# Optimization experiments

Hardware: AMD Instinct MI355X
Metric: run time of the kernel (lower is better)

Reference implementation:

```python
import jax, jax.numpy as jnp
import numpy as np

B, S, HID = 2, 2048, 1024
H, KVH = 16, 4           # query heads, kv heads
D = HID // H             # head_dim = 64
G = H // KVH             # group size (n_rep) = 4


def setup_inputs() -> dict:
    key = jax.random.key(0)
    ks = jax.random.split(key, 6)
    x = jax.random.normal(ks[0], (B, S, HID), dtype=jnp.float32)
    # RoPE tables: [S, D], standard theta=10000
    inv_freq = 1.0 / (10000.0 ** (jnp.arange(0, D, 2, dtype=jnp.float32) / D))
    freqs = jnp.arange(S, dtype=jnp.float32)[:, None] * inv_freq[None, :]  # [S, D/2]
    emb = jnp.concatenate([freqs, freqs], axis=-1)  # [S, D]
    cos, sin = jnp.cos(emb), jnp.sin(emb)
    scale = 0.02
    wq = jax.random.normal(ks[1], (HID, H * D), dtype=jnp.float32) * scale
    wk = jax.random.normal(ks[2], (HID, KVH * D), dtype=jnp.float32) * scale
    wv = jax.random.normal(ks[3], (HID, KVH * D), dtype=jnp.float32) * scale
    wo = jax.random.normal(ks[4], (H * D, HID), dtype=jnp.float32) * scale
    return {"x": x, "cos": cos, "sin": sin, "wq": wq, "wk": wk, "wv": wv, "wo": wo}


def _rotate_half(t):
    h = t.shape[-1] // 2
    return jnp.concatenate([-t[..., h:], t[..., :h]], axis=-1)


def reference(x, cos, sin, wq, wk, wv, wo):
    b, s, _ = x.shape
    q = (x @ wq).reshape(b, s, H, D)
    k = (x @ wk).reshape(b, s, KVH, D)
    v = (x @ wv).reshape(b, s, KVH, D)
    # RoPE (cos/sin broadcast over heads, unsqueeze_dim=1 -> [S,1,D])
    c = cos[:s, None, :]
    sn = sin[:s, None, :]
    q = q * c + _rotate_half(q) * sn
    k = k * c + _rotate_half(k) * sn
    # GQA attention without materializing repeated K/V: group q heads by kv head
    qg = q.reshape(b, s, KVH, G, D)
    scores = jnp.einsum('bqkgd,bskd->bkgqs', qg, k) / jnp.sqrt(jnp.asarray(D, q.dtype))
    causal = jnp.tril(jnp.ones((s, s), dtype=bool))  # [S_q, S_k]
    scores = jnp.where(causal[None, None, None, :, :], scores, -jnp.inf)
    p = jax.nn.softmax(scores, axis=-1)
    out = jnp.einsum('bkgqs,bskd->bqkgd', p, v).reshape(b, s, H * D)
    return out @ wo
```

## Files before the change

### kernel.cpp

```cpp
#include <hip/hip_runtime.h>
#include <hip/hip_bf16.h>


typedef short bfx8 __attribute__((ext_vector_type(8)));
typedef float fx4  __attribute__((ext_vector_type(4)));
typedef float fx16 __attribute__((ext_vector_type(16)));
typedef unsigned int ux4 __attribute__((ext_vector_type(4)));

#define DEV __device__ __forceinline__
#define ALPHA 0.18033688011112042f

DEV void load_lds16(const void* g, void* l) {
  __builtin_amdgcn_global_load_lds(
      (const __attribute__((address_space(1))) unsigned int*)g,
      (__attribute__((address_space(3))) unsigned int*)l, 16, 0, 0);
}

DEV unsigned short f2bf(float f) {
  unsigned int x = __builtin_bit_cast(unsigned int, f);
  unsigned int r = (x + 0x7fffu + ((x >> 16) & 1u)) >> 16;
  return (unsigned short)r;
}
DEV float bf2f(unsigned short u) {
  unsigned int x = ((unsigned int)u) << 16;
  return __builtin_bit_cast(float, x);
}
DEV float exp2_fast(float x) { float r; asm("v_exp_f32 %0, %1" : "=v"(r) : "v"(x)); return r; }
DEV unsigned cvtpk(float lo, float hi) {
  unsigned r; asm("v_cvt_pk_bf16_f32 %0, %1, %2" : "=v"(r) : "v"(lo), "v"(hi)); return r;
}


__global__ __launch_bounds__(256) void cvt_x_kernel(const float* __restrict__ x,
                                                    unsigned short* __restrict__ out) {
  int i = (blockIdx.x * 256 + threadIdx.x) * 8;
  fx4 a = *(const fx4*)(x + i);
  fx4 b = *(const fx4*)(x + i + 4);
  bfx8 r;
  r[0] = (short)f2bf(a[0]); r[1] = (short)f2bf(a[1]);
  r[2] = (short)f2bf(a[2]); r[3] = (short)f2bf(a[3]);
  r[4] = (short)f2bf(b[0]); r[5] = (short)f2bf(b[1]);
  r[6] = (short)f2bf(b[2]); r[7] = (short)f2bf(b[3]);
  *(bfx8*)(out + i) = r;
}


__global__ __launch_bounds__(256) void twqkv_kernel(const float* __restrict__ wq,
                                                    const float* __restrict__ wk,
                                                    const float* __restrict__ wv,
                                                    unsigned short* __restrict__ out) {
  __shared__ float tile[64 * 65];
  const int r0 = blockIdx.x * 64;
  const int c0 = blockIdx.y * 64;
  const float* src; int ncols, rofs;
  if (r0 < 1024)      { src = wq; ncols = 1024; rofs = r0; }
  else if (r0 < 1280) { src = wk; ncols = 256;  rofs = r0 - 1024; }
  else                { src = wv; ncols = 256;  rofs = r0 - 1280; }
  const int t = threadIdx.x;
#pragma unroll
  for (int p = 0; p < 4; ++p) {
    int idx = p * 256 + t;
    int cc = idx >> 4, q4 = idx & 15;
    fx4 v = *(const fx4*)(src + (size_t)(c0 + cc) * ncols + rofs + q4 * 4);
#pragma unroll
    for (int i = 0; i < 4; ++i) tile[(q4 * 4 + i) * 65 + cc] = v[i];
  }
  __syncthreads();
#pragma unroll
  for (int p = 0; p < 2; ++p) {
    int idx = p * 256 + t;
    int rr = idx >> 3, c8 = idx & 7;
    bfx8 v8;
#pragma unroll
    for (int i = 0; i < 8; ++i) v8[i] = (short)f2bf(tile[rr * 65 + c8 * 8 + i]);
    *(bfx8*)(out + (size_t)(r0 + rr) * 1024 + c0 + c8 * 8) = v8;
  }
}

__global__ __launch_bounds__(256) void two_kernel(const float* __restrict__ wo,
                                                  unsigned short* __restrict__ out) {
  __shared__ float tile[64 * 65];
  const int r0 = blockIdx.x * 64, c0 = blockIdx.y * 64;
  const int t = threadIdx.x;
#pragma unroll
  for (int p = 0; p < 4; ++p) {
    int idx = p * 256 + t;
    int cc = idx >> 4, q4 = idx & 15;
    fx4 v = *(const fx4*)(wo + (size_t)(c0 + cc) * 1024 + r0 + q4 * 4);
#pragma unroll
    for (int i = 0; i < 4; ++i) tile[(q4 * 4 + i) * 65 + cc] = v[i];
  }
  __syncthreads();
#pragma unroll
  for (int p = 0; p < 2; ++p) {
    int idx = p * 256 + t;
    int rr = idx >> 3, c8 = idx & 7;
    bfx8 v8;
#pragma unroll
    for (int i = 0; i < 8; ++i) v8[i] = (short)f2bf(tile[rr * 65 + c8 * 8 + i]);
    *(bfx8*)(out + (size_t)(r0 + rr) * 1024 + c0 + c8 * 8) = v8;
  }
}


__global__ __launch_bounds__(256) void vt_kernel(const unsigned short* __restrict__ qkv,
                                                 unsigned short* __restrict__ vT) {
  __shared__ __align__(16) unsigned short tile[64][72];
  const int sc = blockIdx.x;
  const int kvh = blockIdx.y, b = blockIdx.z;
  const int t = threadIdx.x;
  const unsigned short* src = qkv + ((size_t)b * 2048 + sc * 64) * 1536 + 1280 + kvh * 64;
#pragma unroll
  for (int p = 0; p < 2; ++p) {
    int idx = p * 256 + t;
    int row = idx >> 3, c = idx & 7;
    *(bfx8*)(&tile[row][c * 8]) = *(const bfx8*)(src + (size_t)row * 1536 + c * 8);
  }
  __syncthreads();
  unsigned short* dst = vT + ((size_t)(b * 4 + kvh) * 64) * 2048 + sc * 64;
#pragma unroll
  for (int p = 0; p < 2; ++p) {
    int idx = p * 256 + t;
    int d = idx >> 3, c = idx & 7;
    bfx8 v;
#pragma unroll
    for (int i = 0; i < 8; ++i) v[i] = (short)tile[c * 8 + i][d];
    *(bfx8*)(dst + (size_t)d * 2048 + c * 8) = v;
  }
}


template <bool OUT_BF16, bool FUSE_ROPE>
__global__ __launch_bounds__(256) void gemm_bt_kernel(const unsigned short* __restrict__ A,
                                                      const unsigned short* __restrict__ Bt,
                                                      void* __restrict__ Cp,
                                                      int M, int N, int K, int ldc,
                                                      const float* __restrict__ ct,
                                                      const float* __restrict__ st) {
  __shared__ __align__(16) unsigned short As[128 * 32];
  __shared__ __align__(16) unsigned short Bs[128 * 32];
  const int t = threadIdx.x;
  const int l = t & 63;
  const int w = t >> 6;
  const int wm = (w >> 1) * 64, wn = (w & 1) * 64;
  const int bm = blockIdx.x, bn = blockIdx.y;
  fx4 acc[4][4] = {};

  const int ra = t >> 2;
  const int ca = t & 3;

  for (int kt = 0; kt < K; kt += 32) {
    __syncthreads();
#pragma unroll
    for (int p = 0; p < 2; ++p) {
      int rr = ra + p * 64;
      int gca = ((ca ^ ((rr >> 1) & 3)) * 8);
      load_lds16(A + (size_t)(bm * 128 + rr) * K + kt + gca, (char*)As + p * 4096 + t * 16);
      load_lds16(Bt + (size_t)(bn * 128 + rr) * K + kt + gca, (char*)Bs + p * 4096 + t * 16);
    }
    __syncthreads();

    bfx8 af[4], bfr[4];
#pragma unroll
    for (int mi = 0; mi < 4; ++mi) {
      int row = wm + mi * 16 + (l & 15);
      int ch = (l >> 4) ^ ((row >> 1) & 3);
      af[mi] = *(const bfx8*)(As + row * 32 + ch * 8);
      int rowb = wn + mi * 16 + (l & 15);
      int chb = (l >> 4) ^ ((rowb >> 1) & 3);
      bfr[mi] = *(const bfx8*)(Bs + rowb * 32 + chb * 8);
    }
#pragma unroll
    for (int mi = 0; mi < 4; ++mi)
#pragma unroll
      for (int ni = 0; ni < 4; ++ni)
        acc[mi][ni] = __builtin_amdgcn_mfma_f32_16x16x32_bf16(af[mi], bfr[ni], acc[mi][ni], 0, 0, 0);
  }

  const int colbase = bn * 128 + wn;
  if (FUSE_ROPE && colbase < 1280) {
    const float qsc = (colbase < 1024) ? ALPHA : 1.0f;
    unsigned short* Cb = (unsigned short*)Cp;
#pragma unroll
    for (int mi = 0; mi < 4; ++mi) {
      int row0 = bm * 128 + wm + mi * 16 + (l >> 4) * 4;
#pragma unroll
      for (int r = 0; r < 4; ++r) {
        int row = row0 + r, s = row & 2047;
#pragma unroll
        for (int ni = 0; ni < 2; ++ni) {
          int d = ni * 16 + (l & 15);
          float c = ct[s * 64 + d], sn = st[s * 64 + d];
          float x0 = acc[mi][ni][r], x1 = acc[mi][ni + 2][r];
          Cb[(size_t)row * ldc + colbase + d]      = f2bf((x0 * c - x1 * sn) * qsc);
          Cb[(size_t)row * ldc + colbase + d + 32] = f2bf((x1 * c + x0 * sn) * qsc);
        }
      }
    }
  } else {
#pragma unroll
    for (int mi = 0; mi < 4; ++mi) {
      int row0 = bm * 128 + wm + mi * 16 + (l >> 4) * 4;
#pragma unroll
      for (int ni = 0; ni < 4; ++ni) {
        int col = colbase + ni * 16 + (l & 15);
#pragma unroll
        for (int r = 0; r < 4; ++r) {
          if (OUT_BF16)
            ((unsigned short*)Cp)[(size_t)(row0 + r) * ldc + col] = f2bf(acc[mi][ni][r]);
          else
            ((float*)Cp)[(size_t)(row0 + r) * ldc + col] = acc[mi][ni][r];
        }
      }
    }
  }
}


struct Frag { bfx8 kf[4]; bfx8 vf[4]; };

__global__ __launch_bounds__(64) void attn_kernel(const unsigned short* __restrict__ qkv,
                                                  const unsigned short* __restrict__ vT,
                                                  unsigned short* __restrict__ out) {
  __shared__ unsigned Ost[32 * 33];
  const int fid = blockIdx.x;
  const int pid = fid & 31;
  const int uu = fid >> 5;
  const int head = uu & 15, b = uu >> 4;
  const int kvh = head >> 2;
  const int l = threadIdx.x, q5 = l & 31, h = l >> 5;
  const size_t bbase = (size_t)b * 2048;
  const unsigned short* base = qkv + bbase * 1536;
  const unsigned short* kptr = base + 1024 + kvh * 64 + (size_t)q5 * 1536 + 8 * h;
  const unsigned short* vptr = vT + ((size_t)(b * 4 + kvh) * 64 + q5) * 2048 + 8 * h;

  Frag fA, fB;

#define LOADF(F, KB) do {                                                        \
    const unsigned short* kq = kptr + (size_t)(KB) * (32 * 1536);                \
    F.kf[0] = *(const bfx8*)(kq);                                                \
    F.kf[1] = *(const bfx8*)(kq + 16);                                           \
    F.kf[2] = *(const bfx8*)(kq + 32);                                           \
    F.kf[3] = *(const bfx8*)(kq + 48);                                           \
    const unsigned short* vq = vptr + (KB) * 32;                                 \
    F.vf[0] = *(const bfx8*)(vq);                                                \
    F.vf[1] = *(const bfx8*)(vq + 32 * 2048);                                    \
    F.vf[2] = *(const bfx8*)(vq + 16);                                           \
    F.vf[3] = *(const bfx8*)(vq + 16 + 32 * 2048);                               \
  } while (0)

#define STEP(F, KB) do {                                                         \
    fx16 s = {};                                                                 \
    s = __builtin_amdgcn_mfma_f32_32x32x16_bf16(F.kf[0], qf[0], s, 0, 0, 0);     \
    s = __builtin_amdgcn_mfma_f32_32x32x16_bf16(F.kf[1], qf[1], s, 0, 0, 0);     \
    s = __builtin_amdgcn_mfma_f32_32x32x16_bf16(F.kf[2], qf[2], s, 0, 0, 0);     \
    s = __builtin_amdgcn_mfma_f32_32x32x16_bf16(F.kf[3], qf[3], s, 0, 0, 0);     \
    if ((KB) == Tp) {                                                            \
      _Pragma("unroll")                                                          \
      for (int r = 0; r < 16; ++r) {                                             \
        int kr = (r & 3) + 8 * (r >> 2) + 4 * h;                                 \
        if (kr > q5) s[r] = -1e30f;                                              \
      }                                                                          \
    }                                                                            \
    float pmax = s[0];                                                           \
    _Pragma("unroll")                                                            \
    for (int r = 1; r < 16; ++r) pmax = fmaxf(pmax, s[r]);                       \
    pmax = fmaxf(pmax, __shfl_xor(pmax, 32, 64));                                \
    if (!__all(pmax <= mrun + 8.0f)) {                                           \
      float mnew = fmaxf(mrun, pmax);                                            \
      float corr = exp2_fast(mrun - mnew);                                       \
      mrun = mnew;                                                               \
      lrun *= corr;                                                              \
      o[0] *= corr; o[1] *= corr;                                                \
    }                                                                            \
    float lt = 0.f;                                                              \
    _Pragma("unroll")                                                            \
    for (int r = 0; r < 16; ++r) { float pv = exp2_fast(s[r] - mrun); s[r] = pv; lt += pv; } \
    lt += __shfl_xor(lt, 32, 64);                                                \
    lrun += lt;                                                                  \
    unsigned U[8];                                                               \
    _Pragma("unroll")                                                            \
    for (int k8 = 0; k8 < 8; ++k8) U[k8] = cvtpk(s[2 * k8], s[2 * k8 + 1]);      \
    _Pragma("unroll")                                                            \
    for (int kc = 0; kc < 2; ++kc) {                                             \
      unsigned send0 = h ? U[4 * kc] : U[4 * kc + 2];                            \
      unsigned send1 = h ? U[4 * kc + 1] : U[4 * kc + 3];                        \
      unsigned r0 = (unsigned)__shfl_xor((int)send0, 32, 64);                    \
      unsigned r1 = (unsigned)__shfl_xor((int)send1, 32, 64);                    \
      unsigned k0 = h ? U[4 * kc + 2] : U[4 * kc];                               \
      unsigned k1 = h ? U[4 * kc + 3] : U[4 * kc + 1];                           \
      ux4 fr;                                                                    \
      fr[0] = h ? r0 : k0; fr[1] = h ? r1 : k1;                                  \
      fr[2] = h ? k0 : r0; fr[3] = h ? k1 : r1;                                  \
      bfx8 pf = __builtin_bit_cast(bfx8, fr);                                    \
      o[0] = __builtin_amdgcn_mfma_f32_32x32x16_bf16(F.vf[kc * 2], pf, o[0], 0, 0, 0);     \
      o[1] = __builtin_amdgcn_mfma_f32_32x32x16_bf16(F.vf[kc * 2 + 1], pf, o[1], 0, 0, 0); \
    }                                                                            \
  } while (0)

#pragma unroll 1
  for (int sel = 0; sel < 2; ++sel) {
    const int Tp = sel ? (63 - pid) : pid;
    const int q0 = Tp * 32;
    const int nkb = Tp + 1;

    bfx8 qf[4];
#pragma unroll
    for (int dd = 0; dd < 4; ++dd)
      qf[dd] = *(const bfx8*)(base + (size_t)(q0 + q5) * 1536 + head * 64 + dd * 16 + 8 * h);

    fx16 o[2] = {};
    float mrun = -1e30f, lrun = 0.f;

    LOADF(fA, 0);
    int kb = 0;
    while (true) {
      if (kb + 1 < nkb) LOADF(fB, kb + 1);
      STEP(fA, kb);
      ++kb; if (kb >= nkb) break;
      if (kb + 1 < nkb) LOADF(fA, kb + 1);
      STEP(fB, kb);
      ++kb; if (kb >= nkb) break;
    }

    __syncthreads();
    float inv = 1.0f / lrun;
#pragma unroll
    for (int dt = 0; dt < 2; ++dt)
#pragma unroll
      for (int rp = 0; rp < 8; ++rp) {
        int r = 2 * rp;
        float a = o[dt][r] * inv, bb = o[dt][r + 1] * inv;
        int d = 32 * dt + (r & 3) + 8 * (r >> 2) + 4 * h;
        Ost[q5 * 33 + (d >> 1)] = cvtpk(a, bb);
      }
    __syncthreads();
    {
      int rr = l >> 1, half = l & 1;
      const unsigned* src = Ost + rr * 33 + half * 16;
      unsigned short* dst = out + (bbase + q0 + rr) * 1024 + head * 64 + half * 32;
#pragma unroll
      for (int u2 = 0; u2 < 4; ++u2) {
        ux4 v4;
        v4[0] = src[4 * u2]; v4[1] = src[4 * u2 + 1];
        v4[2] = src[4 * u2 + 2]; v4[3] = src[4 * u2 + 3];
        *(ux4*)(dst + u2 * 8) = v4;
      }
    }
  }
#undef LOADF
#undef STEP
}


extern "C" void kernel_launch(void* const* d_in, const int* in_sizes, int n_in,
                              void* d_out, int out_size, void* d_ws, size_t ws_size,
                              hipStream_t stream) {
  const float* x    = (const float*)d_in[0];
  const float* cosb = (const float*)d_in[1];
  const float* sinb = (const float*)d_in[2];
  const float* wq   = (const float*)d_in[3];
  const float* wk   = (const float*)d_in[4];
  const float* wv   = (const float*)d_in[5];
  const float* wo   = (const float*)d_in[6];
  float* out = (float*)d_out;

  char* ws = (char*)d_ws;
  unsigned short* xb    = (unsigned short*)ws;
  unsigned short* attn  = (unsigned short*)ws;
  unsigned short* wqkvT = (unsigned short*)(ws + 8388608);
  unsigned short* vT    = (unsigned short*)(ws + 8388608);
  unsigned short* woT   = (unsigned short*)(ws + 11534336);
  unsigned short* qkv   = (unsigned short*)(ws + 13631488);

  cvt_x_kernel<<<2048, 256, 0, stream>>>(x, xb);
  twqkv_kernel<<<dim3(24, 16), 256, 0, stream>>>(wq, wk, wv, wqkvT);
  two_kernel<<<dim3(16, 16), 256, 0, stream>>>(wo, woT);
  gemm_bt_kernel<true, true><<<dim3(32, 12), 256, 0, stream>>>(xb, wqkvT, qkv, 4096, 1536, 1024, 1536, cosb, sinb);
  vt_kernel<<<dim3(32, 4, 2), 256, 0, stream>>>(qkv, vT);
  attn_kernel<<<1024, 64, 0, stream>>>(qkv, vT, attn);
  gemm_bt_kernel<false, false><<<dim3(32, 8), 256, 0, stream>>>(attn, woT, out, 4096, 1024, 1024, 1024, nullptr, nullptr);
}
```

Before: 210.2 us.

## Fuse weight transposes, write V transposed from QKV GEMM, restructure attention blocks

Merges the two weight-transpose kernels into one launch. The QKV GEMM epilogue now writes V directly in transposed layout, which removes the separate vt kernel and shrinks the qkv row stride to 1280. GEMM tiles are halved in M (64x128) to double the grid. Attention now runs one query tile per workgroup, 2048 workgroups in heaviest-first order, processes 64-key blocks with two score accumulators and s_setprio around MFMAs, and drops a barrier. The risks are more workgroups with less reuse per block and higher register pressure in attention.

```diff
diff --git a/kernel.cpp b/kernel.cpp
--- a/kernel.cpp
+++ b/kernel.cpp
@@ -2,6 +2,7 @@
 #include <hip/hip_bf16.h>
 
 
+typedef short bfx4 __attribute__((ext_vector_type(4)));
 typedef short bfx8 __attribute__((ext_vector_type(8)));
 typedef float fx4  __attribute__((ext_vector_type(4)));
 typedef float fx16 __attribute__((ext_vector_type(16)));
@@ -21,14 +22,11 @@
   unsigned int r = (x + 0x7fffu + ((x >> 16) & 1u)) >> 16;
   return (unsigned short)r;
 }
-DEV float bf2f(unsigned short u) {
-  unsigned int x = ((unsigned int)u) << 16;
-  return __builtin_bit_cast(float, x);
-}
 DEV float exp2_fast(float x) { float r; asm("v_exp_f32 %0, %1" : "=v"(r) : "v"(x)); return r; }
 DEV unsigned cvtpk(float lo, float hi) {
   unsigned r; asm("v_cvt_pk_bf16_f32 %0, %1, %2" : "=v"(r) : "v"(lo), "v"(hi)); return r;
 }
+#define MFMA32 __builtin_amdgcn_mfma_f32_32x32x16_bf16
 
 
 __global__ __launch_bounds__(256) void cvt_x_kernel(const float* __restrict__ x,
@@ -45,17 +43,24 @@
 }
 
 
-__global__ __launch_bounds__(256) void twqkv_kernel(const float* __restrict__ wq,
-                                                    const float* __restrict__ wk,
-                                                    const float* __restrict__ wv,
-                                                    unsigned short* __restrict__ out) {
+__global__ __launch_bounds__(256) void tw_kernel(const float* __restrict__ wq,
+                                                 const float* __restrict__ wk,
+                                                 const float* __restrict__ wv,
+                                                 const float* __restrict__ wo,
+                                                 unsigned short* __restrict__ wqkvT,
+                                                 unsigned short* __restrict__ woT) {
   __shared__ float tile[64 * 65];
-  const int r0 = blockIdx.x * 64;
+  const int bx = blockIdx.x;
   const int c0 = blockIdx.y * 64;
-  const float* src; int ncols, rofs;
-  if (r0 < 1024)      { src = wq; ncols = 1024; rofs = r0; }
-  else if (r0 < 1280) { src = wk; ncols = 256;  rofs = r0 - 1024; }
-  else                { src = wv; ncols = 256;  rofs = r0 - 1280; }
+  const float* src; int ncols, rofs, r0; unsigned short* dst;
+  if (bx < 24) {
+    r0 = bx * 64; dst = wqkvT;
+    if (r0 < 1024)      { src = wq; ncols = 1024; rofs = r0; }
+    else if (r0 < 1280) { src = wk; ncols = 256;  rofs = r0 - 1024; }
+    else                { src = wv; ncols = 256;  rofs = r0 - 1280; }
+  } else {
+    r0 = (bx - 24) * 64; dst = woT; src = wo; ncols = 1024; rofs = r0;
+  }
   const int t = threadIdx.x;
 #pragma unroll
   for (int p = 0; p < 4; ++p) {
@@ -73,59 +78,7 @@
     bfx8 v8;
 #pragma unroll
     for (int i = 0; i < 8; ++i) v8[i] = (short)f2bf(tile[rr * 65 + c8 * 8 + i]);
-    *(bfx8*)(out + (size_t)(r0 + rr) * 1024 + c0 + c8 * 8) = v8;
-  }
-}
-
-__global__ __launch_bounds__(256) void two_kernel(const float* __restrict__ wo,
-                                                  unsigned short* __restrict__ out) {
-  __shared__ float tile[64 * 65];
-  const int r0 = blockIdx.x * 64, c0 = blockIdx.y * 64;
-  const int t = threadIdx.x;
-#pragma unroll
-  for (int p = 0; p < 4; ++p) {
-    int idx = p * 256 + t;
-    int cc = idx >> 4, q4 = idx & 15;
-    fx4 v = *(const fx4*)(wo + (size_t)(c0 + cc) * 1024 + r0 + q4 * 4);
-#pragma unroll
-    for (int i = 0; i < 4; ++i) tile[(q4 * 4 + i) * 65 + cc] = v[i];
-  }
-  __syncthreads();
-#pragma unroll
-  for (int p = 0; p < 2; ++p) {
-    int idx = p * 256 + t;
-    int rr = idx >> 3, c8 = idx & 7;
-    bfx8 v8;
-#pragma unroll
-    for (int i = 0; i < 8; ++i) v8[i] = (short)f2bf(tile[rr * 65 + c8 * 8 + i]);
-    *(bfx8*)(out + (size_t)(r0 + rr) * 1024 + c0 + c8 * 8) = v8;
-  }
-}
-
-
-__global__ __launch_bounds__(256) void vt_kernel(const unsigned short* __restrict__ qkv,
-                                                 unsigned short* __restrict__ vT) {
-  __shared__ __align__(16) unsigned short tile[64][72];
-  const int sc = blockIdx.x;
-  const int kvh = blockIdx.y, b = blockIdx.z;
-  const int t = threadIdx.x;
-  const unsigned short* src = qkv + ((size_t)b * 2048 + sc * 64) * 1536 + 1280 + kvh * 64;
-#pragma unroll
-  for (int p = 0; p < 2; ++p) {
-    int idx = p * 256 + t;
-    int row = idx >> 3, c = idx & 7;
-    *(bfx8*)(&tile[row][c * 8]) = *(const bfx8*)(src + (size_t)row * 1536 + c * 8);
-  }
-  __syncthreads();
-  unsigned short* dst = vT + ((size_t)(b * 4 + kvh) * 64) * 2048 + sc * 64;
-#pragma unroll
-  for (int p = 0; p < 2; ++p) {
-    int idx = p * 256 + t;
-    int d = idx >> 3, c = idx & 7;
-    bfx8 v;
-#pragma unroll
-    for (int i = 0; i < 8; ++i) v[i] = (short)tile[c * 8 + i][d];
-    *(bfx8*)(dst + (size_t)d * 2048 + c * 8) = v;
+    *(bfx8*)(dst + (size_t)(r0 + rr) * 1024 + c0 + c8 * 8) = v8;
   }
 }
 
@@ -134,44 +87,50 @@
 __global__ __launch_bounds__(256) void gemm_bt_kernel(const unsigned short* __restrict__ A,
                                                       const unsigned short* __restrict__ Bt,
                                                       void* __restrict__ Cp,
-                                                      int M, int N, int K, int ldc,
+                                                      int K, int ldc,
                                                       const float* __restrict__ ct,
-                                                      const float* __restrict__ st) {
-  __shared__ __align__(16) unsigned short As[128 * 32];
+                                                      const float* __restrict__ st,
+                                                      unsigned short* __restrict__ vTout) {
+  __shared__ __align__(16) unsigned short As[64 * 32];
   __shared__ __align__(16) unsigned short Bs[128 * 32];
   const int t = threadIdx.x;
   const int l = t & 63;
   const int w = t >> 6;
-  const int wm = (w >> 1) * 64, wn = (w & 1) * 64;
+  const int wm = (w >> 1) * 32, wn = (w & 1) * 64;
   const int bm = blockIdx.x, bn = blockIdx.y;
-  fx4 acc[4][4] = {};
-
-  const int ra = t >> 2;
-  const int ca = t & 3;
+  fx4 acc[2][4] = {};
 
   for (int kt = 0; kt < K; kt += 32) {
     __syncthreads();
+    {
+      int rr = t >> 2, ca = t & 3;
+      int gca = ((ca ^ ((rr >> 1) & 3)) * 8);
+      load_lds16(A + (size_t)(bm * 64 + rr) * K + kt + gca, (char*)As + t * 16);
+    }
 #pragma unroll
     for (int p = 0; p < 2; ++p) {
-      int rr = ra + p * 64;
+      int idx = p * 256 + t;
+      int rr = idx >> 2, ca = idx & 3;
       int gca = ((ca ^ ((rr >> 1) & 3)) * 8);
-      load_lds16(A + (size_t)(bm * 128 + rr) * K + kt + gca, (char*)As + p * 4096 + t * 16);
-      load_lds16(Bt + (size_t)(bn * 128 + rr) * K + kt + gca, (char*)Bs + p * 4096 + t * 16);
+      load_lds16(Bt + (size_t)(bn * 128 + rr) * K + kt + gca, (char*)Bs + idx * 16);
     }
     __syncthreads();
 
-    bfx8 af[4], bfr[4];
-#pragma unroll
-    for (int mi = 0; mi < 4; ++mi) {
+    bfx8 af[2], bfr[4];
+#pragma unroll
+    for (int mi = 0; mi < 2; ++mi) {
       int row = wm + mi * 16 + (l & 15);
       int ch = (l >> 4) ^ ((row >> 1) & 3);
       af[mi] = *(const bfx8*)(As + row * 32 + ch * 8);
-      int rowb = wn + mi * 16 + (l & 15);
+    }
+#pragma unroll
+    for (int ni = 0; ni < 4; ++ni) {
+      int rowb = wn + ni * 16 + (l & 15);
       int chb = (l >> 4) ^ ((rowb >> 1) & 3);
-      bfr[mi] = *(const bfx8*)(Bs + rowb * 32 + chb * 8);
-    }
-#pragma unroll
-    for (int mi = 0; mi < 4; ++mi)
+      bfr[ni] = *(const bfx8*)(Bs + rowb * 32 + chb * 8);
+    }
+#pragma unroll
+    for (int mi = 0; mi < 2; ++mi)
 #pragma unroll
       for (int ni = 0; ni < 4; ++ni)
         acc[mi][ni] = __builtin_amdgcn_mfma_f32_16x16x32_bf16(af[mi], bfr[ni], acc[mi][ni], 0, 0, 0);
@@ -182,8 +141,8 @@
     const float qsc = (colbase < 1024) ? ALPHA : 1.0f;
     unsigned short* Cb = (unsigned short*)Cp;
 #pragma unroll
-    for (int mi = 0; mi < 4; ++mi) {
-      int row0 = bm * 128 + wm + mi * 16 + (l >> 4) * 4;
+    for (int mi = 0; mi < 2; ++mi) {
+      int row0 = bm * 64 + wm + mi * 16 + (l >> 4) * 4;
 #pragma unroll
       for (int r = 0; r < 4; ++r) {
         int row = row0 + r, s = row & 2047;
@@ -192,15 +151,31 @@
           int d = ni * 16 + (l & 15);
           float c = ct[s * 64 + d], sn = st[s * 64 + d];
           float x0 = acc[mi][ni][r], x1 = acc[mi][ni + 2][r];
-          Cb[(size_t)row * ldc + colbase + d]      = f2bf((x0 * c - x1 * sn) * qsc);
-          Cb[(size_t)row * ldc + colbase + d + 32] = f2bf((x1 * c + x0 * sn) * qsc);
+          Cb[(size_t)row * 1280 + colbase + d]      = f2bf((x0 * c - x1 * sn) * qsc);
+          Cb[(size_t)row * 1280 + colbase + d + 32] = f2bf((x1 * c + x0 * sn) * qsc);
         }
       }
     }
+  } else if (FUSE_ROPE) {
+    const int b4 = (bm >> 5) * 4;
+#pragma unroll
+    for (int mi = 0; mi < 2; ++mi) {
+      int row0 = bm * 64 + wm + mi * 16 + (l >> 4) * 4;
+      int s0r = row0 & 2047;
+#pragma unroll
+      for (int ni = 0; ni < 4; ++ni) {
+        int vcol = colbase + ni * 16 + (l & 15) - 1280;
+        int kvh = vcol >> 6, d = vcol & 63;
+        bfx4 pv;
+#pragma unroll
+        for (int r = 0; r < 4; ++r) pv[r] = (short)f2bf(acc[mi][ni][r]);
+        *(bfx4*)(vTout + ((size_t)(b4 + kvh) * 64 + d) * 2048 + s0r) = pv;
+      }
+    }
   } else {
 #pragma unroll
-    for (int mi = 0; mi < 4; ++mi) {
-      int row0 = bm * 128 + wm + mi * 16 + (l >> 4) * 4;
+    for (int mi = 0; mi < 2; ++mi) {
+      int row0 = bm * 64 + wm + mi * 16 + (l >> 4) * 4;
 #pragma unroll
       for (int ni = 0; ni < 4; ++ni) {
         int col = colbase + ni * 16 + (l & 15);
@@ -217,54 +192,82 @@
 }
 
 
-struct Frag { bfx8 kf[4]; bfx8 vf[4]; };
-
-__global__ __launch_bounds__(64) void attn_kernel(const unsigned short* __restrict__ qkv,
-                                                  const unsigned short* __restrict__ vT,
-                                                  unsigned short* __restrict__ out) {
+__global__ __launch_bounds__(64, 2) void attn_kernel(const unsigned short* __restrict__ qkv,
+                                                     const unsigned short* __restrict__ vT,
+                                                     unsigned short* __restrict__ out) {
   __shared__ unsigned Ost[32 * 33];
   const int fid = blockIdx.x;
-  const int pid = fid & 31;
-  const int uu = fid >> 5;
-  const int head = uu & 15, b = uu >> 4;
+  const int Tp = 63 - (fid >> 5);
+  const int hb = fid & 31;
+  const int head = hb & 15, b = hb >> 4;
   const int kvh = head >> 2;
   const int l = threadIdx.x, q5 = l & 31, h = l >> 5;
+  const int q0 = Tp * 32;
+  const int nkb = (Tp >> 1) + 1;
   const size_t bbase = (size_t)b * 2048;
-  const unsigned short* base = qkv + bbase * 1536;
-  const unsigned short* kptr = base + 1024 + kvh * 64 + (size_t)q5 * 1536 + 8 * h;
+  const unsigned short* base = qkv + bbase * 1280;
+  const unsigned short* kptr = base + 1024 + kvh * 64 + (size_t)q5 * 1280 + 8 * h;
   const unsigned short* vptr = vT + ((size_t)(b * 4 + kvh) * 64 + q5) * 2048 + 8 * h;
 
-  Frag fA, fB;
-
-#define LOADF(F, KB) do {                                                        \
-    const unsigned short* kq = kptr + (size_t)(KB) * (32 * 1536);                \
-    F.kf[0] = *(const bfx8*)(kq);                                                \
-    F.kf[1] = *(const bfx8*)(kq + 16);                                           \
-    F.kf[2] = *(const bfx8*)(kq + 32);                                           \
-    F.kf[3] = *(const bfx8*)(kq + 48);                                           \
-    const unsigned short* vq = vptr + (KB) * 32;                                 \
-    F.vf[0] = *(const bfx8*)(vq);                                                \
-    F.vf[1] = *(const bfx8*)(vq + 32 * 2048);                                    \
-    F.vf[2] = *(const bfx8*)(vq + 16);                                           \
-    F.vf[3] = *(const bfx8*)(vq + 16 + 32 * 2048);                               \
+  bfx8 qf[4];
+#pragma unroll
+  for (int dd = 0; dd < 4; ++dd)
+    qf[dd] = *(const bfx8*)(base + (size_t)(q0 + q5) * 1280 + head * 64 + dd * 16 + 8 * h);
+
+  fx16 o[2] = {};
+  float mrun = -1e30f, lrun = 0.f;
+  bfx8 kfA[8], kfB[8], va[8];
+
+#define LOADK(KF, KB) do {                                                       \
+    const unsigned short* kq = kptr + (size_t)((KB) * 64) * 1280;                \
+    KF[0] = *(const bfx8*)(kq);                                                  \
+    KF[1] = *(const bfx8*)(kq + 16);                                             \
+    KF[2] = *(const bfx8*)(kq + 32);                                             \
+    KF[3] = *(const bfx8*)(kq + 48);                                             \
+    const unsigned short* kq1 = kq + 32 * 1280;                                  \
+    KF[4] = *(const bfx8*)(kq1);                                                 \
+    KF[5] = *(const bfx8*)(kq1 + 16);                                            \
+    KF[6] = *(const bfx8*)(kq1 + 32);                                            \
+    KF[7] = *(const bfx8*)(kq1 + 48);                                            \
   } while (0)
 
-#define STEP(F, KB) do {                                                         \
-    fx16 s = {};                                                                 \
-    s = __builtin_amdgcn_mfma_f32_32x32x16_bf16(F.kf[0], qf[0], s, 0, 0, 0);     \
-    s = __builtin_amdgcn_mfma_f32_32x32x16_bf16(F.kf[1], qf[1], s, 0, 0, 0);     \
-    s = __builtin_amdgcn_mfma_f32_32x32x16_bf16(F.kf[2], qf[2], s, 0, 0, 0);     \
-    s = __builtin_amdgcn_mfma_f32_32x32x16_bf16(F.kf[3], qf[3], s, 0, 0, 0);     \
-    if ((KB) == Tp) {                                                            \
+#define LOADV(KB) do {                                                           \
+    const unsigned short* vq = vptr + (KB) * 64;                                 \
+    va[0] = *(const bfx8*)(vq);                                                  \
+    va[1] = *(const bfx8*)(vq + 16);                                             \
+    va[2] = *(const bfx8*)(vq + 32);                                             \
+    va[3] = *(const bfx8*)(vq + 48);                                             \
+    const unsigned short* vq1 = vq + 32 * 2048;                                  \
+    va[4] = *(const bfx8*)(vq1);                                                 \
+    va[5] = *(const bfx8*)(vq1 + 16);                                            \
+    va[6] = *(const bfx8*)(vq1 + 32);                                            \
+    va[7] = *(const bfx8*)(vq1 + 48);                                            \
+  } while (0)
+
+#define STEP(KF, KB) do {                                                        \
+    fx16 s0 = {}, s1 = {};                                                       \
+    __builtin_amdgcn_s_setprio(1);                                               \
+    s0 = MFMA32(KF[0], qf[0], s0, 0, 0, 0);                                      \
+    s1 = MFMA32(KF[4], qf[0], s1, 0, 0, 0);                                      \
+    s0 = MFMA32(KF[1], qf[1], s0, 0, 0, 0);                                      \
+    s1 = MFMA32(KF[5], qf[1], s1, 0, 0, 0);                                      \
+    s0 = MFMA32(KF[2], qf[2], s0, 0, 0, 0);                                      \
+    s1 = MFMA32(KF[6], qf[2], s1, 0, 0, 0);                                      \
+    s0 = MFMA32(KF[3], qf[3], s0, 0, 0, 0);                                      \
+    s1 = MFMA32(KF[7], qf[3], s1, 0, 0, 0);                                      \
+    __builtin_amdgcn_s_setprio(0);                                               \
+    if ((KB) == nkb - 1) {                                                       \
+      const int j0s = (KB) * 64;                                                 \
       _Pragma("unroll")                                                          \
       for (int r = 0; r < 16; ++r) {                                             \
-        int kr = (r & 3) + 8 * (r >> 2) + 4 * h;                                 \
-        if (kr > q5) s[r] = -1e30f;                                              \
+        int key0 = j0s + (r & 3) + 8 * (r >> 2) + 4 * h;                         \
+        if (key0 > q0 + q5) s0[r] = -1e30f;                                      \
+        if (key0 + 32 > q0 + q5) s1[r] = -1e30f;                                 \
       }                                                                          \
     }                                                                            \
-    float pmax = s[0];                                                           \
+    float pmax = fmaxf(s0[0], s1[0]);                                            \
     _Pragma("unroll")                                                            \
-    for (int r = 1; r < 16; ++r) pmax = fmaxf(pmax, s[r]);                       \
+    for (int r = 1; r < 16; ++r) pmax = fmaxf(pmax, fmaxf(s0[r], s1[r]));        \
     pmax = fmaxf(pmax, __shfl_xor(pmax, 32, 64));                                \
     if (!__all(pmax <= mrun + 8.0f)) {                                           \
       float mnew = fmaxf(mrun, pmax);                                            \
@@ -273,83 +276,82 @@
       lrun *= corr;                                                              \
       o[0] *= corr; o[1] *= corr;                                                \
     }                                                                            \
-    float lt = 0.f;                                                              \
+    float lt0 = 0.f, lt1 = 0.f;                                                  \
     _Pragma("unroll")                                                            \
-    for (int r = 0; r < 16; ++r) { float pv = exp2_fast(s[r] - mrun); s[r] = pv; lt += pv; } \
+    for (int r = 0; r < 16; ++r) {                                               \
+      float p0 = exp2_fast(s0[r] - mrun); s0[r] = p0; lt0 += p0;                 \
+      float p1 = exp2_fast(s1[r] - mrun); s1[r] = p1; lt1 += p1;                 \
+    }                                                                            \
+    float lt = lt0 + lt1;                                                        \
     lt += __shfl_xor(lt, 32, 64);                                                \
     lrun += lt;                                                                  \
-    unsigned U[8];                                                               \
+    unsigned U[2][8];                                                            \
     _Pragma("unroll")                                                            \
-    for (int k8 = 0; k8 < 8; ++k8) U[k8] = cvtpk(s[2 * k8], s[2 * k8 + 1]);      \
+    for (int k8 = 0; k8 < 8; ++k8) {                                             \
+      U[0][k8] = cvtpk(s0[2 * k8], s0[2 * k8 + 1]);                              \
+      U[1][k8] = cvtpk(s1[2 * k8], s1[2 * k8 + 1]);                              \
+    }                                                                            \
     _Pragma("unroll")                                                            \
-    for (int kc = 0; kc < 2; ++kc) {                                             \
-      unsigned send0 = h ? U[4 * kc] : U[4 * kc + 2];                            \
-      unsigned send1 = h ? U[4 * kc + 1] : U[4 * kc + 3];                        \
-      unsigned r0 = (unsigned)__shfl_xor((int)send0, 32, 64);                    \
-      unsigned r1 = (unsigned)__shfl_xor((int)send1, 32, 64);                    \
-      unsigned k0 = h ? U[4 * kc + 2] : U[4 * kc];                               \
-      unsigned k1 = h ? U[4 * kc + 3] : U[4 * kc + 1];                           \
-      ux4 fr;                                                                    \
-      fr[0] = h ? r0 : k0; fr[1] = h ? r1 : k1;                                  \
-      fr[2] = h ? k0 : r0; fr[3] = h ? k1 : r1;                                  \
-      bfx8 pf = __builtin_bit_cast(bfx8, fr);                                    \
-      o[0] = __builtin_amdgcn_mfma_f32_32x32x16_bf16(F.vf[kc * 2], pf, o[0], 0, 0, 0);     \
-      o[1] = __builtin_amdgcn_mfma_f32_32x32x16_bf16(F.vf[kc * 2 + 1], pf, o[1], 0, 0, 0); \
+    for (int hs = 0; hs < 2; ++hs) {                                             \
+      _Pragma("unroll")                                                          \
+      for (int e = 0; e < 2; ++e) {                                              \
+        unsigned send0 = h ? U[hs][4 * e] : U[hs][4 * e + 2];                    \
+        unsigned send1 = h ? U[hs][4 * e + 1] : U[hs][4 * e + 3];                \
+        unsigned r0 = (unsigned)__shfl_xor((int)send0, 32, 64);                  \
+        unsigned r1 = (unsigned)__shfl_xor((int)send1, 32, 64);                  \
+        unsigned k0 = h ? U[hs][4 * e + 2] : U[hs][4 * e];                       \
+        unsigned k1 = h ? U[hs][4 * e + 3] : U[hs][4 * e + 1];                   \
+        ux4 fr;                                                                  \
+        fr[0] = h ? r0 : k0; fr[1] = h ? r1 : k1;                                \
+        fr[2] = h ? k0 : r0; fr[3] = h ? k1 : r1;                                \
+        bfx8 pf = __builtin_bit_cast(bfx8, fr);                                  \
+        __builtin_amdgcn_s_setprio(1);                                           \
+        o[0] = MFMA32(va[2 * hs + e], pf, o[0], 0, 0, 0);                        \
+        o[1] = MFMA32(va[4 + 2 * hs + e], pf, o[1], 0, 0, 0);                    \
+        __builtin_amdgcn_s_setprio(0);                                           \
+      }                                                                          \
     }                                                                            \
   } while (0)
 
-#pragma unroll 1
-  for (int sel = 0; sel < 2; ++sel) {
-    const int Tp = sel ? (63 - pid) : pid;
-    const int q0 = Tp * 32;
-    const int nkb = Tp + 1;
-
-    bfx8 qf[4];
-#pragma unroll
-    for (int dd = 0; dd < 4; ++dd)
-      qf[dd] = *(const bfx8*)(base + (size_t)(q0 + q5) * 1536 + head * 64 + dd * 16 + 8 * h);
-
-    fx16 o[2] = {};
-    float mrun = -1e30f, lrun = 0.f;
-
-    LOADF(fA, 0);
-    int kb = 0;
-    while (true) {
-      if (kb + 1 < nkb) LOADF(fB, kb + 1);
-      STEP(fA, kb);
-      ++kb; if (kb >= nkb) break;
-      if (kb + 1 < nkb) LOADF(fA, kb + 1);
-      STEP(fB, kb);
-      ++kb; if (kb >= nkb) break;
-    }
-
-    __syncthreads();
-    float inv = 1.0f / lrun;
-#pragma unroll
-    for (int dt = 0; dt < 2; ++dt)
-#pragma unroll
-      for (int rp = 0; rp < 8; ++rp) {
-        int r = 2 * rp;
-        float a = o[dt][r] * inv, bb = o[dt][r + 1] * inv;
-        int d = 32 * dt + (r & 3) + 8 * (r >> 2) + 4 * h;
-        Ost[q5 * 33 + (d >> 1)] = cvtpk(a, bb);
-      }
-    __syncthreads();
-    {
-      int rr = l >> 1, half = l & 1;
-      const unsigned* src = Ost + rr * 33 + half * 16;
-      unsigned short* dst = out + (bbase + q0 + rr) * 1024 + head * 64 + half * 32;
-#pragma unroll
-      for (int u2 = 0; u2 < 4; ++u2) {
-        ux4 v4;
-        v4[0] = src[4 * u2]; v4[1] = src[4 * u2 + 1];
-        v4[2] = src[4 * u2 + 2]; v4[3] = src[4 * u2 + 3];
-        *(ux4*)(dst + u2 * 8) = v4;
-      }
-    }
-  }
-#undef LOADF
+  LOADK(kfA, 0);
+  int kb = 0;
+  while (true) {
+    LOADV(kb);
+    if (kb + 1 < nkb) LOADK(kfB, kb + 1);
+    STEP(kfA, kb);
+    ++kb; if (kb >= nkb) break;
+    LOADV(kb);
+    if (kb + 1 < nkb) LOADK(kfA, kb + 1);
+    STEP(kfB, kb);
+    ++kb; if (kb >= nkb) break;
+  }
+#undef LOADK
+#undef LOADV
 #undef STEP
+
+  float inv = 1.0f / lrun;
+#pragma unroll
+  for (int dt = 0; dt < 2; ++dt)
+#pragma unroll
+    for (int rp = 0; rp < 8; ++rp) {
+      int r = 2 * rp;
+      int d = 32 * dt + (r & 3) + 8 * (r >> 2) + 4 * h;
+      Ost[q5 * 33 + (d >> 1)] = cvtpk(o[dt][r] * inv, o[dt][r + 1] * inv);
+    }
+  asm volatile("s_waitcnt lgkmcnt(0)" ::: "memory");
+  __builtin_amdgcn_sched_barrier(0);
+  {
+    int rr = l >> 1, half = l & 1;
+    const unsigned* src = Ost + rr * 33 + half * 16;
+    unsigned short* dst = out + (bbase + q0 + rr) * 1024 + head * 64 + half * 32;
+#pragma unroll
+    for (int u2 = 0; u2 < 4; ++u2) {
+      ux4 v4;
+      v4[0] = src[4 * u2]; v4[1] = src[4 * u2 + 1];
+      v4[2] = src[4 * u2 + 2]; v4[3] = src[4 * u2 + 3];
+      *(ux4*)(dst + u2 * 8) = v4;
+    }
+  }
 }
 
 
@@ -369,15 +371,13 @@
   unsigned short* xb    = (unsigned short*)ws;
   unsigned short* attn  = (unsigned short*)ws;
   unsigned short* wqkvT = (unsigned short*)(ws + 8388608);
-  unsigned short* vT    = (unsigned short*)(ws + 8388608);
   unsigned short* woT   = (unsigned short*)(ws + 11534336);
   unsigned short* qkv   = (unsigned short*)(ws + 13631488);
+  unsigned short* vT    = (unsigned short*)(ws + 24117248);
 
   cvt_x_kernel<<<2048, 256, 0, stream>>>(x, xb);
-  twqkv_kernel<<<dim3(24, 16), 256, 0, stream>>>(wq, wk, wv, wqkvT);
-  two_kernel<<<dim3(16, 16), 256, 0, stream>>>(wo, woT);
-  gemm_bt_kernel<true, true><<<dim3(32, 12), 256, 0, stream>>>(xb, wqkvT, qkv, 4096, 1536, 1024, 1536, cosb, sinb);
-  vt_kernel<<<dim3(32, 4, 2), 256, 0, stream>>>(qkv, vT);
-  attn_kernel<<<1024, 64, 0, stream>>>(qkv, vT, attn);
-  gemm_bt_kernel<false, false><<<dim3(32, 8), 256, 0, stream>>>(attn, woT, out, 4096, 1024, 1024, 1024, nullptr, nullptr);
-}
+  tw_kernel<<<dim3(40, 16), 256, 0, stream>>>(wq, wk, wv, wo, wqkvT, woT);
+  gemm_bt_kernel<true, true><<<dim3(64, 12), 256, 0, stream>>>(xb, wqkvT, qkv, 1024, 1280, cosb, sinb, vT);
+  attn_kernel<<<2048, 64, 0, stream>>>(qkv, vT, attn);
+  gemm_bt_kernel<false, false><<<dim3(64, 8), 256, 0, stream>>>(attn, woT, out, 1024, 1024, nullptr, nullptr, nullptr);
+}
```

Measured after the change: 203.6 us. -3.1%, faster.
